# Performance work log

Hardware: AMD Instinct MI355X
Metric: run time of the kernel (lower is better)

## Reference

```python
import jax, jax.numpy as jnp
import numpy as np

B = 262144
N_MAX = 4
N_EXPERTS = sum(n * n for n in range(1, N_MAX + 1))  # 30
# offset of expert block for each n (experts within n indexed by l*l + l + m)
OFFSETS = np.cumsum([0] + [n * n for n in range(1, N_MAX)])  # [0,1,5,14]


def _expert_id(n, l, m):
    off = jnp.asarray(OFFSETS, dtype=jnp.int32)
    return off[n - 1] + l * l + l + m  # (B,) int


def setup_inputs() -> dict:
    key = jax.random.key(0)
    ks = jax.random.split(key, 12)
    x = jax.random.normal(ks[0], (B, 3), dtype=jnp.float32)
    # valid coupled quantum numbers: 1<=n<=4, 0<=l<n, -l<=m<=l
    n = jax.random.randint(ks[1], (B,), 1, N_MAX + 1)
    ul = jax.random.uniform(ks[2], (B,))
    l = jnp.floor(ul * n.astype(jnp.float32)).astype(jnp.int32)
    l = jnp.clip(l, 0, n - 1)
    um = jax.random.uniform(ks[3], (B,))
    m = jnp.floor(um * (2 * l + 1).astype(jnp.float32)).astype(jnp.int32) - l
    m = jnp.clip(m, -l, l)
    s = 0.1
    W0 = jax.random.normal(ks[4], (3, 128), dtype=jnp.float32) * s
    b0 = jnp.zeros((128,), dtype=jnp.float32)
    W1 = jax.random.normal(ks[5], (128, 64), dtype=jnp.float32) * s
    b1 = jnp.zeros((64,), dtype=jnp.float32)
    Wa = jax.random.normal(ks[6], (N_EXPERTS, 64, 32), dtype=jnp.float32) * s
    ba = jax.random.normal(ks[7], (N_EXPERTS, 32), dtype=jnp.float32) * s
    Wb = jax.random.normal(ks[8], (N_EXPERTS, 32, 2), dtype=jnp.float32) * s
    bb = jax.random.normal(ks[9], (N_EXPERTS, 2), dtype=jnp.float32) * s
    return {"x": x, "n": n.astype(jnp.int32), "l": l, "m": m,
            "W0": W0, "b0": b0, "W1": W1, "b1": b1,
            "Wa": Wa, "ba": ba, "Wb": Wb, "bb": bb}


def reference(x, n, l, m, W0, b0, W1, b1, Wa, ba, Wb, bb):
    eid = _expert_id(n, l, m)  # (B,)
    # shared trunk (dropout is identity in eval mode)
    h = jnp.tanh(x @ W0 + b0)          # (B,128)
    h = jnp.tanh(h @ W1 + b1)          # (B,64)
    # per-sample expert dispatch via irregular gather of tiny MLP weights
    g = jnp.tanh(jnp.einsum('bd,bdh->bh', h, Wa[eid]) + ba[eid])  # (B,32)
    psi = jnp.einsum('bh,bho->bo', g, Wb[eid]) + bb[eid]          # (B,2)
    norm = jnp.sqrt(jnp.sum(psi * psi, axis=1, keepdims=True) + 1e-6)
    return psi / norm
```

## Files before the change

### kernel.cpp

```cpp
#include <hip/hip_runtime.h>
#include <math.h>


#define THREADS 64
#define NE 30
#define HB 1024
#define MAXBLK 4126
#define SA 67
#define SG 36

typedef short bf16x8 __attribute__((ext_vector_type(8)));
typedef float f32x4 __attribute__((ext_vector_type(4)));

__device__ __forceinline__ int expert_id(int nn, int ll, int mm) {
    return ((nn - 1) * nn * (2 * nn - 1)) / 6 + ll * ll + ll + mm;
}

__device__ __forceinline__ float fast_tanh(float v) {
    float e = __builtin_exp2f(v * 2.885390082f);
    return fmaf(-2.0f, __builtin_amdgcn_rcpf(e + 1.0f), 1.0f);
}

__device__ __forceinline__ unsigned int f2b(float f) {
    unsigned int u = __float_as_uint(f);
    return (u + 0x7fffu + ((u >> 16) & 1u)) >> 16;
}
__device__ __forceinline__ float b2f(unsigned int b) {
    return __uint_as_float(b << 16);
}
__device__ __forceinline__ unsigned int packsplit(float v) {
    const unsigned int hb = f2b(v);
    const float lo = v - b2f(hb);
    return (__float_as_uint(lo) & 0xffff0000u) | hb;
}

union U8 { unsigned int u[4]; bf16x8 v; };
__device__ __forceinline__ void unpack8(const unsigned int* w, bf16x8& hi, bf16x8& lo) {
    U8 H, L;
#pragma unroll
    for (int i = 0; i < 4; ++i) {
        H.u[i] = __builtin_amdgcn_perm(w[2 * i + 1], w[2 * i], 0x05040100u);
        L.u[i] = __builtin_amdgcn_perm(w[2 * i + 1], w[2 * i], 0x07060302u);
    }
    hi = H.v; lo = L.v;
}

__global__ void hist_pack_kernel(const int* __restrict__ nq, const int* __restrict__ lq,
                                 const int* __restrict__ mq,
                                 int* __restrict__ eids, int* __restrict__ etot,
                                 int* __restrict__ bbase,
                                 const float* __restrict__ W1,
                                 unsigned short* __restrict__ W1fh, unsigned short* __restrict__ W1fl,
                                 const float* __restrict__ Wa,
                                 unsigned short* __restrict__ Wafh, unsigned short* __restrict__ Wafl,
                                 int B) {
    const int tid = threadIdx.x;
    const int bx = blockIdx.x;
    if (bx < HB) {
        __shared__ int h[NE];
        if (tid < NE) h[tid] = 0;
        __syncthreads();
        const int per = B / HB, base = bx * per;
        for (int i = tid; i < per; i += blockDim.x) {
            const int e = expert_id(nq[base + i], lq[base + i], mq[base + i]);
            eids[base + i] = e;
            atomicAdd(&h[e], 1);
        }
        __syncthreads();
        if (tid < NE) bbase[bx * NE + tid] = atomicAdd(&etot[tid], h[tid]);
    } else if (bx == HB) {
        for (int i = tid; i < 8192; i += blockDim.x) {
            const int j = i & 7, s = (i >> 3) & 15, q = (i >> 7) & 3;
            const int nt = (i >> 9) & 3, c = i >> 11;
            const int k = c * 32 + q * 8 + j, n = nt * 16 + s;
            const float w = W1[k * 64 + n];
            const unsigned int hb = f2b(w);
            W1fh[i] = (unsigned short)hb;
            W1fl[i] = (unsigned short)f2b(w - b2f(hb));
        }
    } else {
        const int e = bx - HB - 1;
        for (int i = tid; i < 2048; i += blockDim.x) {
            const int j = i & 7, s = (i >> 3) & 15, q = (i >> 7) & 3;
            const int nt2 = (i >> 9) & 1, c2 = (i >> 10) & 1;
            const int d = c2 * 32 + q * 8 + j, hh = nt2 * 16 + s;
            const float w = Wa[e * 2048 + d * 32 + hh];
            const unsigned int hb = f2b(w);
            Wafh[e * 2048 + i] = (unsigned short)hb;
            Wafl[e * 2048 + i] = (unsigned short)f2b(w - b2f(hb));
        }
    }
}

__global__ void scatter_kernel(const int* __restrict__ eids, const int* __restrict__ etot,
                               const int* __restrict__ bbase, int* __restrict__ perm,
                               int4* __restrict__ desc, int B) {
    const int tid = threadIdx.x;
    if (blockIdx.x == HB) {
        __shared__ int es[NE], tq[NE], pb[NE + 1];
        if (tid == 0) {
            int e0 = 0, c = 0;
            for (int e = 0; e < NE; ++e) {
                const int t = etot[e];
                es[e] = e0; tq[e] = t; pb[e] = c;
                c += (t + THREADS - 1) >> 6;
                e0 += t;
            }
            pb[NE] = c;
        }
        __syncthreads();
        const int tot = pb[NE];
        for (int b = tid; b < MAXBLK; b += blockDim.x) {
            int4 d = make_int4(-1, 0, 0, 0);
            if (b < tot) {
                int e = 0;
                while (pb[e + 1] <= b) ++e;
                const int seg = b - pb[e];
                d.x = e;
                d.y = es[e] + (seg << 6);
                d.z = min(THREADS, tq[e] - (seg << 6));
            }
            desc[b] = d;
        }
        return;
    }
    __shared__ int lcnt[NE], esrt[NE], bb[NE];
    if (tid < NE) { lcnt[tid] = 0; bb[tid] = bbase[blockIdx.x * NE + tid]; }
    if (tid == 0) {
        int es0 = 0;
        for (int e = 0; e < NE; ++e) { esrt[e] = es0; es0 += etot[e]; }
    }
    __syncthreads();
    const int per = B / HB;
    const int blk = blockIdx.x * per;
    for (int i = tid; i < per; i += blockDim.x) {
        const int idx = blk + i;
        const int e = eids[idx];
        const int r = atomicAdd(&lcnt[e], 1);
        perm[esrt[e] + bb[e] + r] = idx;
    }
}

__global__ __launch_bounds__(THREADS, 4) void wfc_kernel(
    const float* __restrict__ x, const int* __restrict__ perm,
    const int4* __restrict__ desc,
    const float* __restrict__ W0, const float* __restrict__ b0,
    const bf16x8* __restrict__ W1fh, const bf16x8* __restrict__ W1fl,
    const float* __restrict__ b1,
    const bf16x8* __restrict__ Wafh, const bf16x8* __restrict__ Wafl,
    const float* __restrict__ ba,
    const float* __restrict__ Wb, const float* __restrict__ bb,
    float* __restrict__ out)
{
    __shared__ unsigned int sbuf[2304];

    const int4 dsc = desc[blockIdx.x];
    if (dsc.x < 0) return;
    const int eid  = __builtin_amdgcn_readfirstlane(dsc.x);
    const int start = dsc.y;
    const int cnt   = dsc.z;

    const int tid = threadIdx.x;
    const bool valid = tid < cnt;
    const int idx = perm[start + (valid ? tid : 0)];

    const int lane = tid & 63;
    const int wv   = tid >> 6;
    const int qd   = lane >> 4;
    const int l16  = lane & 15;

    const float x0 = x[idx * 3 + 0];
    const float x1 = x[idx * 3 + 1];
    const float x2 = x[idx * 3 + 2];

    f32x4 acc[4][4];
#pragma unroll
    for (int nt = 0; nt < 4; ++nt) {
        const float bv = b1[nt * 16 + l16];
#pragma unroll
        for (int mt = 0; mt < 4; ++mt) {
            f32x4 c; c[0] = bv; c[1] = bv; c[2] = bv; c[3] = bv;
            acc[mt][nt] = c;
        }
    }

    for (int c = 0; c < 4; ++c) {
        if (c) __syncthreads();
#pragma unroll
        for (int kk = 0; kk < 32; ++kk) {
            const int k = c * 32 + kk;
            const float pre = fmaf(x0, W0[k], fmaf(x1, W0[128 + k], fmaf(x2, W0[256 + k], b0[k])));
            sbuf[kk * SA + tid] = packsplit(fast_tanh(pre));
        }
        __syncthreads();

        bf16x8 Bhi[4], Blo[4];
#pragma unroll
        for (int nt = 0; nt < 4; ++nt) {
            const int rec = (c * 4 + nt) * 64 + qd * 16 + l16;
            Bhi[nt] = W1fh[rec];
            Blo[nt] = W1fl[rec];
        }
#pragma unroll
        for (int mt = 0; mt < 4; ++mt) {
            unsigned int a[8];
            const int mrow = wv * 64 + mt * 16 + l16;
#pragma unroll
            for (int j = 0; j < 8; ++j) a[j] = sbuf[(qd * 8 + j) * SA + mrow];
            bf16x8 Ahi, Alo;
            unpack8(a, Ahi, Alo);
#pragma unroll
            for (int nt = 0; nt < 4; ++nt) {
                acc[mt][nt] = __builtin_amdgcn_mfma_f32_16x16x32_bf16(Ahi, Bhi[nt], acc[mt][nt], 0, 0, 0);
                acc[mt][nt] = __builtin_amdgcn_mfma_f32_16x16x32_bf16(Ahi, Blo[nt], acc[mt][nt], 0, 0, 0);
                acc[mt][nt] = __builtin_amdgcn_mfma_f32_16x16x32_bf16(Alo, Bhi[nt], acc[mt][nt], 0, 0, 0);
            }
        }
    }

    f32x4 acc2[4][2];
#pragma unroll
    for (int nt2 = 0; nt2 < 2; ++nt2) {
        const float bv = ba[(eid << 5) + nt2 * 16 + l16];
#pragma unroll
        for (int mt = 0; mt < 4; ++mt) {
            f32x4 c; c[0] = bv; c[1] = bv; c[2] = bv; c[3] = bv;
            acc2[mt][nt2] = c;
        }
    }

    const bf16x8* __restrict__ waeh = Wafh + (eid << 8);
    const bf16x8* __restrict__ wael = Wafl + (eid << 8);
    for (int c2 = 0; c2 < 2; ++c2) {
        __syncthreads();
#pragma unroll
        for (int mt = 0; mt < 4; ++mt) {
#pragma unroll
            for (int ntl = 0; ntl < 2; ++ntl) {
#pragma unroll
                for (int r = 0; r < 4; ++r) {
                    const float h2 = fast_tanh(acc[mt][c2 * 2 + ntl][r]);
                    const int dl  = ntl * 16 + l16;
                    const int row = wv * 64 + mt * 16 + qd * 4 + r;
                    sbuf[dl * SA + row] = packsplit(h2);
                }
            }
        }
        __syncthreads();

        bf16x8 B2hi[2], B2lo[2];
#pragma unroll
        for (int nt2 = 0; nt2 < 2; ++nt2) {
            const int rec = (c2 * 2 + nt2) * 64 + qd * 16 + l16;
            B2hi[nt2] = waeh[rec];
            B2lo[nt2] = wael[rec];
        }
#pragma unroll
        for (int mt = 0; mt < 4; ++mt) {
            unsigned int a[8];
            const int mrow = wv * 64 + mt * 16 + l16;
#pragma unroll
            for (int j = 0; j < 8; ++j) a[j] = sbuf[(qd * 8 + j) * SA + mrow];
            bf16x8 Ahi, Alo;
            unpack8(a, Ahi, Alo);
#pragma unroll
            for (int nt2 = 0; nt2 < 2; ++nt2) {
                acc2[mt][nt2] = __builtin_amdgcn_mfma_f32_16x16x32_bf16(Ahi, B2hi[nt2], acc2[mt][nt2], 0, 0, 0);
                acc2[mt][nt2] = __builtin_amdgcn_mfma_f32_16x16x32_bf16(Ahi, B2lo[nt2], acc2[mt][nt2], 0, 0, 0);
                acc2[mt][nt2] = __builtin_amdgcn_mfma_f32_16x16x32_bf16(Alo, B2hi[nt2], acc2[mt][nt2], 0, 0, 0);
            }
        }
    }

    __syncthreads();
    float* g2 = (float*)sbuf;
#pragma unroll
    for (int mt = 0; mt < 4; ++mt) {
#pragma unroll
        for (int nt2 = 0; nt2 < 2; ++nt2) {
#pragma unroll
            for (int r = 0; r < 4; ++r) {
                const int row = wv * 64 + mt * 16 + qd * 4 + r;
                g2[row * SG + nt2 * 16 + l16] = fast_tanh(acc2[mt][nt2][r]);
            }
        }
    }
    __syncthreads();

    float gv[32];
    {
        const float4* grow = (const float4*)(g2 + tid * SG);
#pragma unroll
        for (int i = 0; i < 8; ++i) {
            float4 v = grow[i];
            gv[4 * i + 0] = v.x; gv[4 * i + 1] = v.y;
            gv[4 * i + 2] = v.z; gv[4 * i + 3] = v.w;
        }
    }

    const float* __restrict__ wbe = Wb + (eid << 6);
    float p0 = bb[2 * eid], p1 = bb[2 * eid + 1];
#pragma unroll
    for (int h = 0; h < 32; ++h) {
        p0 = fmaf(gv[h], wbe[2 * h + 0], p0);
        p1 = fmaf(gv[h], wbe[2 * h + 1], p1);
    }

    const float s = fmaf(p0, p0, fmaf(p1, p1, 1e-6f));
    const float inv = 1.0f / sqrtf(s);
    if (valid) {
        float2 o; o.x = p0 * inv; o.y = p1 * inv;
        ((float2*)out)[idx] = o;
    }
}

extern "C" void kernel_launch(void* const* d_in, const int* in_sizes, int n_in,
                              void* d_out, int out_size, void* d_ws, size_t ws_size,
                              hipStream_t stream) {
    const float* x  = (const float*)d_in[0];
    const int*   n  = (const int*)d_in[1];
    const int*   l  = (const int*)d_in[2];
    const int*   m  = (const int*)d_in[3];
    const float* W0 = (const float*)d_in[4];
    const float* b0 = (const float*)d_in[5];
    const float* W1 = (const float*)d_in[6];
    const float* b1 = (const float*)d_in[7];
    const float* Wa = (const float*)d_in[8];
    const float* ba = (const float*)d_in[9];
    const float* Wb = (const float*)d_in[10];
    const float* bb = (const float*)d_in[11];
    float* out = (float*)d_out;

    const int B = in_sizes[1];

    int*            perm  = (int*)d_ws;
    int*            eids  = perm + B;
    int*            bbase = eids + B;
    int*            etot  = bbase + HB * NE;
    int4*           desc  = (int4*)(etot + 32);
    unsigned short* W1fh  = (unsigned short*)(desc + MAXBLK);
    unsigned short* W1fl  = W1fh + 8192;
    unsigned short* Wafh  = W1fl + 8192;
    unsigned short* Wafl  = Wafh + NE * 2048;

    hipMemsetAsync(etot, 0, 32 * sizeof(int), stream);
    hist_pack_kernel<<<HB + 1 + NE, 256, 0, stream>>>(
        n, l, m, eids, etot, bbase, W1, W1fh, W1fl, Wa, Wafh, Wafl, B);
    scatter_kernel<<<HB + 1, 256, 0, stream>>>(eids, etot, bbase, perm, desc, B);
    wfc_kernel<<<MAXBLK, THREADS, 0, stream>>>(
        x, perm, desc, W0, b0,
        (const bf16x8*)W1fh, (const bf16x8*)W1fl, b1,
        (const bf16x8*)Wafh, (const bf16x8*)Wafl, ba, Wb, bb, out);
}
```

Before: 155.8 us.

## Reduce histogram blocks and pad global expert counters to avoid atomic contention

Cuts the histogram and scatter grids from 1024 to 256 blocks, each now handling 1024 samples, so there are four times fewer global atomics on the per-expert totals. The totals are spaced 16 ints apart so each expert counter sits on its own cache line, avoiding false sharing between atomics. The scatter kernel now loads the totals into shared memory once instead of reading global memory serially in a loop. PER is hardcoded, which assumes B equals 256*1024, and fewer blocks means less parallelism in these small kernels.

```diff
diff --git a/kernel.cpp b/kernel.cpp
--- a/kernel.cpp
+++ b/kernel.cpp
@@ -4,7 +4,9 @@
 
 #define THREADS 64
 #define NE 30
-#define HB 1024
+#define HB 256
+#define PER 1024
+#define ETS 16
 #define MAXBLK 4126
 #define SA 67
 #define SG 36
@@ -60,14 +62,15 @@
         __shared__ int h[NE];
         if (tid < NE) h[tid] = 0;
         __syncthreads();
-        const int per = B / HB, base = bx * per;
-        for (int i = tid; i < per; i += blockDim.x) {
+        const int base = bx * PER;
+        for (int i = tid; i < PER; i += blockDim.x) {
             const int e = expert_id(nq[base + i], lq[base + i], mq[base + i]);
             eids[base + i] = e;
             atomicAdd(&h[e], 1);
         }
         __syncthreads();
-        if (tid < NE) bbase[bx * NE + tid] = atomicAdd(&etot[tid], h[tid]);
+        if (tid < NE)
+            bbase[bx * NE + tid] = atomicAdd(&etot[tid * ETS], h[tid]);
     } else if (bx == HB) {
         for (int i = tid; i < 8192; i += blockDim.x) {
             const int j = i & 7, s = (i >> 3) & 15, q = (i >> 7) & 3;
@@ -97,14 +100,15 @@
                                int4* __restrict__ desc, int B) {
     const int tid = threadIdx.x;
     if (blockIdx.x == HB) {
-        __shared__ int es[NE], tq[NE], pb[NE + 1];
+        __shared__ int tq[NE], es[NE], pb[NE + 1];
+        if (tid < NE) tq[tid] = etot[tid * ETS];
+        __syncthreads();
         if (tid == 0) {
             int e0 = 0, c = 0;
             for (int e = 0; e < NE; ++e) {
-                const int t = etot[e];
-                es[e] = e0; tq[e] = t; pb[e] = c;
-                c += (t + THREADS - 1) >> 6;
-                e0 += t;
+                es[e] = e0; pb[e] = c;
+                c += (tq[e] + THREADS - 1) >> 6;
+                e0 += tq[e];
             }
             pb[NE] = c;
         }
@@ -124,16 +128,20 @@
         }
         return;
     }
-    __shared__ int lcnt[NE], esrt[NE], bb[NE];
-    if (tid < NE) { lcnt[tid] = 0; bb[tid] = bbase[blockIdx.x * NE + tid]; }
+    __shared__ int lcnt[NE], esrt[NE], bb[NE], tq[NE];
+    if (tid < NE) {
+        lcnt[tid] = 0;
+        bb[tid] = bbase[blockIdx.x * NE + tid];
+        tq[tid] = etot[tid * ETS];
+    }
+    __syncthreads();
     if (tid == 0) {
         int es0 = 0;
-        for (int e = 0; e < NE; ++e) { esrt[e] = es0; es0 += etot[e]; }
+        for (int e = 0; e < NE; ++e) { esrt[e] = es0; es0 += tq[e]; }
     }
     __syncthreads();
-    const int per = B / HB;
-    const int blk = blockIdx.x * per;
-    for (int i = tid; i < per; i += blockDim.x) {
+    const int blk = blockIdx.x * PER;
+    for (int i = tid; i < PER; i += blockDim.x) {
         const int idx = blk + i;
         const int e = eids[idx];
         const int r = atomicAdd(&lcnt[e], 1);
@@ -337,13 +345,13 @@
     int*            eids  = perm + B;
     int*            bbase = eids + B;
     int*            etot  = bbase + HB * NE;
-    int4*           desc  = (int4*)(etot + 32);
+    int4*           desc  = (int4*)(etot + 512);
     unsigned short* W1fh  = (unsigned short*)(desc + MAXBLK);
     unsigned short* W1fl  = W1fh + 8192;
     unsigned short* Wafh  = W1fl + 8192;
     unsigned short* Wafl  = Wafh + NE * 2048;
 
-    hipMemsetAsync(etot, 0, 32 * sizeof(int), stream);
+    hipMemsetAsync(etot, 0, NE * ETS * sizeof(int), stream);
     hist_pack_kernel<<<HB + 1 + NE, 256, 0, stream>>>(
         n, l, m, eids, etot, bbase, W1, W1fh, W1fl, Wa, Wafh, Wafl, B);
     scatter_kernel<<<HB + 1, 256, 0, stream>>>(eids, etot, bbase, perm, desc, B);
```

Result: faster. 147.0 us (-5.6%).
